# Optimization experiments

Measured on AMD Instinct MI355X. Metric: run time of the kernel, lower is better.

## Reference

```python
import jax, jax.numpy as jnp
import numpy as np

N_KERNELS = 5
MUL_FACTOR = 2.0


def setup_inputs() -> dict:
    key = jax.random.key(0)
    k1, k2 = jax.random.split(key)
    X = jax.random.normal(k1, (4096, 512), dtype=jnp.float32)
    Y = jax.random.normal(k2, (4096, 512), dtype=jnp.float32)
    return {"X": X, "Y": Y}


def _mmd(X, Y):
    # multipliers: 2.0 ** (arange(5) - 2) = [0.25, 0.5, 1, 2, 4]
    mults = MUL_FACTOR ** (jnp.arange(N_KERNELS, dtype=jnp.float32) - N_KERNELS // 2)
    Z = jnp.concatenate([X, Y], axis=0)            # [N+M, D]
    n = Z.shape[0]
    # squared euclidean pairwise distances (cdist ** 2)
    sq = jnp.sum(Z * Z, axis=-1)                    # [N+M]
    D2 = sq[:, None] + sq[None, :] - 2.0 * (Z @ Z.T)
    D2 = jnp.maximum(D2, 0.0)                       # [N+M, N+M]
    # bandwidth from detached distances: sum / (n^2 - n)
    bw = jax.lax.stop_gradient(jnp.sum(D2)) / (n * n - n)
    # multi-bandwidth RBF sum over kernels
    K = jnp.sum(jnp.exp(-D2[None, :, :] / (bw * mults)[:, None, None]), axis=0)
    Nx = X.shape[0]
    XX = jnp.mean(K[:Nx, :Nx])
    XY = jnp.mean(K[:Nx, Nx:])
    YY = jnp.mean(K[Nx:, Nx:])
    return XX - 2.0 * XY + YY


def reference(X, Y):
    return _mmd(X, Y)
```

## Files before the change

kernel.cpp:

```cpp
#include <hip/hip_runtime.h>

#define N_ROWS 8192
#define NX     4096
#define DIM    512
#define BT     128
#define NT     64
#define NTRI   2080
#define BK     32
#define NPERS  768

typedef __bf16 bf16_t;
typedef bf16_t bf16x8 __attribute__((ext_vector_type(8)));
typedef float  f32x4  __attribute__((ext_vector_type(4)));

#if __has_builtin(__builtin_amdgcn_exp2f)
  #define EXP2F __builtin_amdgcn_exp2f
#else
  #define EXP2F exp2f
#endif


__device__ __forceinline__ const float* zrow(const float* X, const float* Y, int r) {
    return (r < NX) ? (X + (size_t)r * DIM) : (Y + (size_t)(r - NX) * DIM);
}

__device__ __forceinline__ void gload_lds16(const bf16_t* g, bf16_t* l) {
    __builtin_amdgcn_global_load_lds(
        (__attribute__((address_space(1))) void*)(void*)(g),
        (__attribute__((address_space(3))) void*)(void*)(l), 16, 0, 0);
}

__global__ void k_prep(const float* __restrict__ X, const float* __restrict__ Y,
                       bf16_t* __restrict__ Zh, float* __restrict__ sqrow,
                       float* __restrict__ colsum, unsigned* __restrict__ tk1,
                       double* __restrict__ S1acc) {
    int t = threadIdx.x;
    if (blockIdx.x == 0) {
        colsum[t] = 0.f; colsum[t + 256] = 0.f;
        if (t == 0) { *tk1 = 0u; *S1acc = 0.0; }
    }
    int wv = t >> 6, lane = t & 63;
    int row = blockIdx.x * 4 + wv;
    const float4* z4 = (const float4*)zrow(X, Y, row);
    float4 a = z4[lane * 2], b = z4[lane * 2 + 1];
    bf16x8 h;
    h[0] = (bf16_t)a.x; h[1] = (bf16_t)a.y; h[2] = (bf16_t)a.z; h[3] = (bf16_t)a.w;
    h[4] = (bf16_t)b.x; h[5] = (bf16_t)b.y; h[6] = (bf16_t)b.z; h[7] = (bf16_t)b.w;
    *(bf16x8*)(Zh + (size_t)row * DIM + lane * 8) = h;
    float s = a.x*a.x + a.y*a.y + a.z*a.z + a.w*a.w
            + b.x*b.x + b.y*b.y + b.z*b.z + b.w*b.w;
    #pragma unroll
    for (int off = 32; off > 0; off >>= 1) s += __shfl_down(s, off);
    if (lane == 0) sqrow[row] = s;
}

__global__ __launch_bounds__(512) void k_colsum(const bf16_t* __restrict__ Zh,
                                                const float* __restrict__ sqrow,
                                                float* __restrict__ colsum,
                                                float* __restrict__ cvals,
                                                double* __restrict__ S1acc,
                                                unsigned* __restrict__ tk1,
                                                double* __restrict__ acc,
                                                unsigned* __restrict__ tk2) {
    __shared__ float red[8][4][8];
    __shared__ double dred[512];
    __shared__ int is_last;
    int t = threadIdx.x, lane = t & 63, wv = t >> 6;
    int n16 = lane & 15, q16 = lane >> 4;
    int g = blockIdx.x & 15, slab = blockIdx.x >> 4;
    int c0 = g * 32 + q16 * 8;
    float s[8] = {0.f, 0.f, 0.f, 0.f, 0.f, 0.f, 0.f, 0.f};
    #pragma unroll
    for (int it = 0; it < 8; ++it) {
        int r = slab * 1024 + it * 128 + wv * 16 + n16;
        bf16x8 v = *(const bf16x8*)(Zh + (size_t)r * DIM + c0);
        #pragma unroll
        for (int j = 0; j < 8; ++j) s[j] += (float)v[j];
    }
    #pragma unroll
    for (int off = 8; off >= 1; off >>= 1)
        #pragma unroll
        for (int j = 0; j < 8; ++j) s[j] += __shfl_down(s[j], off);
    if (n16 == 0)
        #pragma unroll
        for (int j = 0; j < 8; ++j) red[wv][q16][j] = s[j];
    __syncthreads();
    float oldc = 0.f;
    if (t < 32) {
        int q = t >> 3, j = t & 7;
        float v = 0.f;
        #pragma unroll
        for (int w = 0; w < 8; ++w) v += red[w][q][j];
        oldc = atomicAdd(&colsum[g * 32 + q * 8 + j], v);
    }
    double olds = 0.0;
    if (g == 0) {
        int i = slab * 1024 + t;
        double d = (double)sqrow[i] + (double)sqrow[i + 512];
        #pragma unroll
        for (int off = 32; off > 0; off >>= 1) d += __shfl_down(d, off);
        if (lane == 0) olds = atomicAdd(S1acc, d);
    }
    asm volatile("" :: "v"(oldc), "v"(olds));
    asm volatile("s_waitcnt vmcnt(0)" ::: "memory");
    __syncthreads();
    if (t == 0) is_last = (atomicAdd(tk1, 1u) == 127u);
    __syncthreads();
    if (!is_last) return;
    float cv = atomicAdd(&colsum[t], 0.f);
    dred[t] = (double)cv * (double)cv;
    __syncthreads();
    for (int off = 256; off > 0; off >>= 1) {
        if (t < off) dred[t] += dred[t + off];
        __syncthreads();
    }
    if (t < 8) acc[t * 16] = 0.0;
    if (t == 0) {
        double S1 = atomicAdd(S1acc, 0.0);
        double n = (double)N_ROWS;
        double sumD2 = 2.0 * n * S1 - 2.0 * dred[0];
        double bw = sumD2 / (n * n - n);
        const double LOG2E = 1.4426950408889634;
        double mult = 0.25;
        for (int k = 0; k < 5; ++k) {
            cvals[k] = (float)(-LOG2E / (bw * mult));
            mult *= 2.0;
        }
        *tk2 = 0u;
    }
}

__global__ __launch_bounds__(256, 3) void k_pair(const bf16_t* __restrict__ Zh,
                                                 const float* __restrict__ sqrow,
                                                 const float* __restrict__ cvals,
                                                 double* __restrict__ acc,
                                                 unsigned* __restrict__ tk2,
                                                 float* __restrict__ out) {
    int b = blockIdx.x;
    int ntile = (b < NTRI - 2 * NPERS) ? 3 : 2;
    int tis[3], tjs[3];
    #pragma unroll
    for (int g = 0; g < 3; ++g) {
        int T = b + g * NPERS;
        int ti_ = 0, tj_ = 0;
        if (T < NTRI) {
            int q = (T & 7) * (NTRI / 8) + (T >> 3);
            int I = 0, rem = q;
            #pragma unroll
            for (int it = 0; it < 8; ++it) {
                int rowcnt = 36 + (7 - I) * 64;
                if (rem >= rowcnt && I < 7) { rem -= rowcnt; ++I; } else break;
            }
            if (rem < 36) {
                int a = 0;
                #pragma unroll
                for (int it = 0; it < 7; ++it) {
                    int nxt = (a + 1) * 8 - (a + 1) * a / 2;
                    if (nxt <= rem) ++a; else break;
                }
                int off = a * 8 - a * (a - 1) / 2;
                ti_ = I * 8 + a;
                tj_ = I * 8 + a + (rem - off);
            } else {
                int r2 = rem - 36;
                int J = I + 1 + (r2 >> 6);
                int w = r2 & 63;
                ti_ = I * 8 + (w >> 3);
                tj_ = J * 8 + (w & 7);
            }
        }
        tis[g] = ti_; tjs[g] = tj_;
    }

    __shared__ bf16_t As[3][4096];
    __shared__ bf16_t Bs[3][4096];
    __shared__ float wsum[4];

    int t = threadIdx.x, lane = t & 63, wv = t >> 6;
    int wr = wv >> 1, wc = wv & 1;
    int n16 = lane & 15, q16 = lane >> 4;

    int r0_, q0_, r1_, q1_;
    { int c0 = t;       r0_ = c0 >> 2; q0_ = (c0 & 3) ^ ((r0_ >> 1) & 3);
      int c1 = 256 + t; r1_ = c1 >> 2; q1_ = (c1 & 3) ^ ((r1_ >> 1) & 3); }
    int ldsoff0 = (wv * 64) * 8;
    int ldsoff1 = (256 + wv * 64) * 8;

    int aoff[4], boff[4];
    #pragma unroll
    for (int aa = 0; aa < 4; ++aa) {
        int r = 16 * (wr * 4 + aa) + n16;
        aoff[aa] = (r * 4 + (q16 ^ ((r >> 1) & 3))) * 8;
    }
    #pragma unroll
    for (int bb = 0; bb < 4; ++bb) {
        int r = 16 * (wc * 4 + bb) + n16;
        boff[bb] = (r * 4 + (q16 ^ ((r >> 1) & 3))) * 8;
    }

    float c4 = cvals[4];

#define SETPTRS(TI, TJ, A0, B0, A1, B1) do {                        \
        (A0) = Zh + (size_t)((TI) * BT + r0_) * DIM + q0_ * 8;      \
        (B0) = Zh + (size_t)((TJ) * BT + r0_) * DIM + q0_ * 8;      \
        (A1) = Zh + (size_t)((TI) * BT + r1_) * DIM + q1_ * 8;      \
        (B1) = Zh + (size_t)((TJ) * BT + r1_) * DIM + q1_ * 8;      \
    } while (0)

#define STAGEP(A0, B0, A1, B1, KN, BUF) do {                        \
        gload_lds16((A0) + (KN), &As[BUF][ldsoff0]);                \
        gload_lds16((B0) + (KN), &Bs[BUF][ldsoff0]);                \
        gload_lds16((A1) + (KN), &As[BUF][ldsoff1]);                \
        gload_lds16((B1) + (KN), &Bs[BUF][ldsoff1]);                \
    } while (0)

#define WAITBAR(VM) do {                                            \
        asm volatile("s_waitcnt vmcnt(" VM ")" ::: "memory");       \
        __builtin_amdgcn_s_barrier();                               \
        __builtin_amdgcn_sched_barrier(0);                          \
    } while (0)

#define DOMFMA(RB) do {                                             \
        const bf16_t* Ab = &As[RB][0];                              \
        const bf16_t* Bb = &Bs[RB][0];                              \
        bf16x8 av[4], bv[4];                                        \
        _Pragma("unroll")                                           \
        for (int aa = 0; aa < 4; ++aa) av[aa] = *(const bf16x8*)(Ab + aoff[aa]); \
        _Pragma("unroll")                                           \
        for (int bb = 0; bb < 4; ++bb) bv[bb] = *(const bf16x8*)(Bb + boff[bb]); \
        __builtin_amdgcn_s_setprio(1);                              \
        _Pragma("unroll")                                           \
        for (int aa = 0; aa < 4; ++aa)                              \
            _Pragma("unroll")                                       \
            for (int bb = 0; bb < 4; ++bb)                          \
                accf[aa][bb] = __builtin_amdgcn_mfma_f32_16x16x32_bf16( \
                    av[aa], bv[bb], accf[aa][bb], 0, 0, 0);         \
        __builtin_amdgcn_s_setprio(0);                              \
    } while (0)

    const bf16_t *cA0, *cB0, *cA1, *cB1;
    SETPTRS(tis[0], tjs[0], cA0, cB0, cA1, cB1);
    STAGEP(cA0, cB0, cA1, cB1, 0, 0);
    STAGEP(cA0, cB0, cA1, cB1, BK, 1);

    #pragma unroll
    for (int g = 0; g < 3; ++g) {
        if (g >= ntile) break;
        int has_next = (g + 1 < ntile);
        const bf16_t *nA0 = cA0, *nB0 = cB0, *nA1 = cA1, *nB1 = cB1;
        if (has_next) SETPTRS(tis[g + 1], tjs[g + 1], nA0, nB0, nA1, nB1);

        f32x4 accf[4][4];
        #pragma unroll
        for (int a = 0; a < 4; ++a)
            #pragma unroll
            for (int bb = 0; bb < 4; ++bb)
                accf[a][bb] = (f32x4){0.f, 0.f, 0.f, 0.f};

        int rb = g % 3;
        const bf16_t *pA0 = cA0 + 2 * BK, *pB0 = cB0 + 2 * BK;
        const bf16_t *pA1 = cA1 + 2 * BK, *pB1 = cB1 + 2 * BK;
        for (int s = 0; s < 14; ++s) {
            WAITBAR("4");
            int wb = rb + 2; if (wb >= 3) wb -= 3;
            STAGEP(pA0, pB0, pA1, pB1, 0, wb);
            pA0 += BK; pB0 += BK; pA1 += BK; pB1 += BK;
            DOMFMA(rb);
            ++rb; if (rb == 3) rb = 0;
        }
        WAITBAR("4");
        if (has_next) STAGEP(nA0, nB0, nA1, nB1, 0, (g + 1) % 3);
        DOMFMA((g + 2) % 3);
        if (has_next) {
            WAITBAR("4");
            STAGEP(nA0, nB0, nA1, nB1, BK, (g + 2) % 3);
        } else {
            WAITBAR("0");
        }
        DOMFMA(g % 3);

        int i0 = tis[g] * BT + wr * 64;
        int j0 = tjs[g] * BT + wc * 64;
        float sqi[4][4], sqj[4];
        #pragma unroll
        for (int aa = 0; aa < 4; ++aa)
            #pragma unroll
            for (int r = 0; r < 4; ++r)
                sqi[aa][r] = sqrow[i0 + 16 * aa + q16 * 4 + r];
        #pragma unroll
        for (int bb = 0; bb < 4; ++bb)
            sqj[bb] = sqrow[j0 + 16 * bb + n16];

        float s_local = 0.f;
        #pragma unroll
        for (int aa = 0; aa < 4; ++aa) {
            #pragma unroll
            for (int bb = 0; bb < 4; ++bb) {
                #pragma unroll
                for (int r = 0; r < 4; ++r) {
                    float d2 = fmaf(-2.f, accf[aa][bb][r], sqi[aa][r] + sqj[bb]);
                    d2 = fmaxf(d2, 0.f);
                    float e4 = EXP2F(d2 * c4);
                    float e3 = e4 * e4;
                    float e2 = e3 * e3;
                    float e1 = e2 * e2;
                    float e0 = e1 * e1;
                    s_local += e4 + e3 + e2 + e1 + e0;
                }
            }
        }
        #pragma unroll
        for (int off = 32; off > 0; off >>= 1) s_local += __shfl_down(s_local, off);
        if (lane == 0) wsum[wv] = s_local;
        __syncthreads();
        if (t == 0) {
            float bs = wsum[0] + wsum[1] + wsum[2] + wsum[3];
            double si = (tis[g] < NT / 2) ? 1.0 : -1.0;
            double sj = (tjs[g] < NT / 2) ? 1.0 : -1.0;
            double w = si * sj * ((tis[g] == tjs[g]) ? 1.0 : 2.0);
            double oldv = atomicAdd(&acc[(b & 7) * 16], w * (double)bs);
            asm volatile("" :: "v"(oldv));
        }
        if (has_next) { cA0 = nA0; cB0 = nB0; cA1 = nA1; cB1 = nB1; }
    }

    if (t == 0) {
        asm volatile("s_waitcnt vmcnt(0)" ::: "memory");
        unsigned old = atomicAdd(tk2, 1u);
        if (old == NPERS - 1) {
            double ssum = 0.0;
            #pragma unroll
            for (int i = 0; i < 8; ++i) ssum += atomicAdd(&acc[i * 16], 0.0);
            out[0] = (float)(ssum / ((double)NX * (double)NX));
        }
    }
#undef SETPTRS
#undef STAGEP
#undef WAITBAR
#undef DOMFMA
}

extern "C" void kernel_launch(void* const* d_in, const int* in_sizes, int n_in,
                              void* d_out, int out_size, void* d_ws, size_t ws_size,
                              hipStream_t stream) {
    const float* X = (const float*)d_in[0];
    const float* Y = (const float*)d_in[1];
    float* out = (float*)d_out;

    float*    sqrow  = (float*)d_ws;
    float*    colsum = sqrow + 8192;
    float*    cvals  = (float*)((char*)d_ws + 34816);
    unsigned* tk1    = (unsigned*)((char*)d_ws + 34840);
    unsigned* tk2    = (unsigned*)((char*)d_ws + 34844);
    double*   S1acc  = (double*)((char*)d_ws + 34848);
    double*   acc    = (double*)((char*)d_ws + 34944);
    bf16_t*   Zh     = (bf16_t*)((char*)d_ws + 36864);

    k_prep  <<<2048, 256, 0, stream>>>(X, Y, Zh, sqrow, colsum, tk1, S1acc);
    k_colsum<<<128, 512, 0, stream>>>(Zh, sqrow, colsum, cvals, S1acc, tk1, acc, tk2);
    k_pair  <<<NPERS, 256, 0, stream>>>(Zh, sqrow, cvals, acc, tk2, out);
}
```

Baseline: 132.2 us.

## Fuse column-sum bandwidth reduction into pair kernel with dynamic tile queue

Removes the separate k_colsum launch and folds its column-sum and bandwidth computation into the first 128 blocks of k_pair. Those blocks publish the exp coefficients through a flag that other blocks spin-wait on before the epilogue, so the GEMM main loop can overlap with the reduction. Static three-tiles-per-block assignment is replaced by an atomic work queue so persistent blocks pull tiles dynamically for better load balance. The cost is extra per-tile atomics and barriers, a spin-wait that depends on all 128 reducer blocks being co-resident, and a possible deadlock if they are not.

```diff
diff --git a/kernel.cpp b/kernel.cpp
--- a/kernel.cpp
+++ b/kernel.cpp
@@ -30,14 +30,42 @@
         (__attribute__((address_space(3))) void*)(void*)(l), 16, 0, 0);
 }
 
+__device__ __forceinline__ void decode_tile(int T, int* pti, int* ptj) {
+    int q = (T & 7) * (NTRI / 8) + (T >> 3);
+    int I = 0, rem = q;
+    #pragma unroll
+    for (int it = 0; it < 8; ++it) {
+        int rowcnt = 36 + (7 - I) * 64;
+        if (rem >= rowcnt && I < 7) { rem -= rowcnt; ++I; } else break;
+    }
+    if (rem < 36) {
+        int a = 0;
+        #pragma unroll
+        for (int it = 0; it < 7; ++it) {
+            int nxt = (a + 1) * 8 - (a + 1) * a / 2;
+            if (nxt <= rem) ++a; else break;
+        }
+        int off = a * 8 - a * (a - 1) / 2;
+        *pti = I * 8 + a;
+        *ptj = I * 8 + a + (rem - off);
+    } else {
+        int r2 = rem - 36;
+        int J = I + 1 + (r2 >> 6);
+        int w = r2 & 63;
+        *pti = I * 8 + (w >> 3);
+        *ptj = J * 8 + (w & 7);
+    }
+}
+
 __global__ void k_prep(const float* __restrict__ X, const float* __restrict__ Y,
                        bf16_t* __restrict__ Zh, float* __restrict__ sqrow,
                        float* __restrict__ colsum, unsigned* __restrict__ tk1,
-                       double* __restrict__ S1acc) {
+                       unsigned* __restrict__ tk2, double* __restrict__ S1acc,
+                       unsigned* __restrict__ wq, unsigned* __restrict__ flag) {
     int t = threadIdx.x;
     if (blockIdx.x == 0) {
         colsum[t] = 0.f; colsum[t + 256] = 0.f;
-        if (t == 0) { *tk1 = 0u; *S1acc = 0.0; }
+        if (t == 0) { *tk1 = 0u; *tk2 = 0u; *S1acc = 0.0; *wq = NPERS; *flag = 0u; }
     }
     int wv = t >> 6, lane = t & 63;
     int row = blockIdx.x * 4 + wv;
@@ -54,138 +82,110 @@
     if (lane == 0) sqrow[row] = s;
 }
 
-__global__ __launch_bounds__(512) void k_colsum(const bf16_t* __restrict__ Zh,
-                                                const float* __restrict__ sqrow,
-                                                float* __restrict__ colsum,
-                                                float* __restrict__ cvals,
-                                                double* __restrict__ S1acc,
-                                                unsigned* __restrict__ tk1,
-                                                double* __restrict__ acc,
-                                                unsigned* __restrict__ tk2) {
-    __shared__ float red[8][4][8];
-    __shared__ double dred[512];
-    __shared__ int is_last;
-    int t = threadIdx.x, lane = t & 63, wv = t >> 6;
-    int n16 = lane & 15, q16 = lane >> 4;
-    int g = blockIdx.x & 15, slab = blockIdx.x >> 4;
-    int c0 = g * 32 + q16 * 8;
-    float s[8] = {0.f, 0.f, 0.f, 0.f, 0.f, 0.f, 0.f, 0.f};
-    #pragma unroll
-    for (int it = 0; it < 8; ++it) {
-        int r = slab * 1024 + it * 128 + wv * 16 + n16;
-        bf16x8 v = *(const bf16x8*)(Zh + (size_t)r * DIM + c0);
-        #pragma unroll
-        for (int j = 0; j < 8; ++j) s[j] += (float)v[j];
-    }
-    #pragma unroll
-    for (int off = 8; off >= 1; off >>= 1)
-        #pragma unroll
-        for (int j = 0; j < 8; ++j) s[j] += __shfl_down(s[j], off);
-    if (n16 == 0)
-        #pragma unroll
-        for (int j = 0; j < 8; ++j) red[wv][q16][j] = s[j];
-    __syncthreads();
-    float oldc = 0.f;
-    if (t < 32) {
-        int q = t >> 3, j = t & 7;
-        float v = 0.f;
-        #pragma unroll
-        for (int w = 0; w < 8; ++w) v += red[w][q][j];
-        oldc = atomicAdd(&colsum[g * 32 + q * 8 + j], v);
-    }
-    double olds = 0.0;
-    if (g == 0) {
-        int i = slab * 1024 + t;
-        double d = (double)sqrow[i] + (double)sqrow[i + 512];
-        #pragma unroll
-        for (int off = 32; off > 0; off >>= 1) d += __shfl_down(d, off);
-        if (lane == 0) olds = atomicAdd(S1acc, d);
-    }
-    asm volatile("" :: "v"(oldc), "v"(olds));
-    asm volatile("s_waitcnt vmcnt(0)" ::: "memory");
-    __syncthreads();
-    if (t == 0) is_last = (atomicAdd(tk1, 1u) == 127u);
-    __syncthreads();
-    if (!is_last) return;
-    float cv = atomicAdd(&colsum[t], 0.f);
-    dred[t] = (double)cv * (double)cv;
-    __syncthreads();
-    for (int off = 256; off > 0; off >>= 1) {
-        if (t < off) dred[t] += dred[t + off];
-        __syncthreads();
-    }
-    if (t < 8) acc[t * 16] = 0.0;
-    if (t == 0) {
-        double S1 = atomicAdd(S1acc, 0.0);
-        double n = (double)N_ROWS;
-        double sumD2 = 2.0 * n * S1 - 2.0 * dred[0];
-        double bw = sumD2 / (n * n - n);
-        const double LOG2E = 1.4426950408889634;
-        double mult = 0.25;
-        for (int k = 0; k < 5; ++k) {
-            cvals[k] = (float)(-LOG2E / (bw * mult));
-            mult *= 2.0;
-        }
-        *tk2 = 0u;
-    }
-}
-
 __global__ __launch_bounds__(256, 3) void k_pair(const bf16_t* __restrict__ Zh,
                                                  const float* __restrict__ sqrow,
-                                                 const float* __restrict__ cvals,
+                                                 float* __restrict__ colsum,
+                                                 float* __restrict__ cvals,
+                                                 double* __restrict__ S1acc,
+                                                 unsigned* __restrict__ tk1,
+                                                 unsigned* __restrict__ wq,
+                                                 unsigned* __restrict__ flag,
                                                  double* __restrict__ acc,
                                                  unsigned* __restrict__ tk2,
                                                  float* __restrict__ out) {
     int b = blockIdx.x;
-    int ntile = (b < NTRI - 2 * NPERS) ? 3 : 2;
-    int tis[3], tjs[3];
-    #pragma unroll
-    for (int g = 0; g < 3; ++g) {
-        int T = b + g * NPERS;
-        int ti_ = 0, tj_ = 0;
-        if (T < NTRI) {
-            int q = (T & 7) * (NTRI / 8) + (T >> 3);
-            int I = 0, rem = q;
-            #pragma unroll
-            for (int it = 0; it < 8; ++it) {
-                int rowcnt = 36 + (7 - I) * 64;
-                if (rem >= rowcnt && I < 7) { rem -= rowcnt; ++I; } else break;
-            }
-            if (rem < 36) {
-                int a = 0;
-                #pragma unroll
-                for (int it = 0; it < 7; ++it) {
-                    int nxt = (a + 1) * 8 - (a + 1) * a / 2;
-                    if (nxt <= rem) ++a; else break;
-                }
-                int off = a * 8 - a * (a - 1) / 2;
-                ti_ = I * 8 + a;
-                tj_ = I * 8 + a + (rem - off);
-            } else {
-                int r2 = rem - 36;
-                int J = I + 1 + (r2 >> 6);
-                int w = r2 & 63;
-                ti_ = I * 8 + (w >> 3);
-                tj_ = J * 8 + (w & 7);
-            }
-        }
-        tis[g] = ti_; tjs[g] = tj_;
-    }
-
     __shared__ bf16_t As[3][4096];
     __shared__ bf16_t Bs[3][4096];
     __shared__ float wsum[4];
+    __shared__ int   lds_next;
+    __shared__ float lds_c4;
 
     int t = threadIdx.x, lane = t & 63, wv = t >> 6;
-    int wr = wv >> 1, wc = wv & 1;
     int n16 = lane & 15, q16 = lane >> 4;
+
+    if (b < 128) {
+        float* red = (float*)&Bs[0][0];
+        double* dred = (double*)&As[0][0];
+        int g = b & 15, slab = b >> 4;
+        int c0 = g * 32 + q16 * 8;
+        float s[8] = {0.f,0.f,0.f,0.f,0.f,0.f,0.f,0.f};
+        for (int it = 0; it < 16; ++it) {
+            int r = slab * 1024 + it * 64 + wv * 16 + n16;
+            bf16x8 v = *(const bf16x8*)(Zh + (size_t)r * DIM + c0);
+            #pragma unroll
+            for (int j = 0; j < 8; ++j) s[j] += (float)v[j];
+        }
+        #pragma unroll
+        for (int off = 8; off >= 1; off >>= 1)
+            #pragma unroll
+            for (int j = 0; j < 8; ++j) s[j] += __shfl_down(s[j], off);
+        if (n16 == 0)
+            #pragma unroll
+            for (int j = 0; j < 8; ++j) red[(wv * 4 + q16) * 8 + j] = s[j];
+        __syncthreads();
+        float oldc = 0.f;
+        if (t < 32) {
+            int q = t >> 3, j = t & 7;
+            float v = 0.f;
+            #pragma unroll
+            for (int w = 0; w < 4; ++w) v += red[(w * 4 + q) * 8 + j];
+            oldc = atomicAdd(&colsum[g * 32 + q * 8 + j], v);
+        }
+        double olds = 0.0;
+        if (g == 0) {
+            int i = slab * 1024 + t;
+            double d = (double)sqrow[i] + (double)sqrow[i + 256]
+                     + (double)sqrow[i + 512] + (double)sqrow[i + 768];
+            #pragma unroll
+            for (int off = 32; off > 0; off >>= 1) d += __shfl_down(d, off);
+            if (lane == 0) olds = atomicAdd(S1acc, d);
+        }
+        asm volatile("" :: "v"(oldc), "v"(olds));
+        asm volatile("s_waitcnt vmcnt(0)" ::: "memory");
+        __syncthreads();
+        __shared__ int is_last;
+        if (t == 0) is_last = (atomicAdd(tk1, 1u) == 127u);
+        __syncthreads();
+        if (is_last) {
+            float cv0 = atomicAdd(&colsum[t], 0.f);
+            float cv1 = atomicAdd(&colsum[t + 256], 0.f);
+            dred[t] = (double)cv0 * cv0 + (double)cv1 * cv1;
+            __syncthreads();
+            for (int off = 128; off > 0; off >>= 1) {
+                if (t < off) dred[t] += dred[t + off];
+                __syncthreads();
+            }
+            if (t < 8) {
+                unsigned long long o =
+                    atomicExch((unsigned long long*)&acc[t * 16], 0ull);
+                asm volatile("" :: "v"(o));
+            }
+            if (t == 0) {
+                double S1 = atomicAdd(S1acc, 0.0);
+                double n = (double)N_ROWS;
+                double bw = (2.0 * n * S1 - 2.0 * dred[0]) / (n * n - n);
+                const double LOG2E = 1.4426950408889634;
+                double mult = 0.25;
+                float olda = 0.f;
+                for (int k = 0; k < 5; ++k) {
+                    olda += atomicExch(&cvals[k], (float)(-LOG2E / (bw * mult)));
+                    mult *= 2.0;
+                }
+                asm volatile("" :: "v"(olda));
+                asm volatile("s_waitcnt vmcnt(0)" ::: "memory");
+                unsigned of = atomicExch(flag, 1u);
+                asm volatile("" :: "v"(of));
+            }
+            __syncthreads();
+        }
+    }
 
     int r0_, q0_, r1_, q1_;
     { int c0 = t;       r0_ = c0 >> 2; q0_ = (c0 & 3) ^ ((r0_ >> 1) & 3);
       int c1 = 256 + t; r1_ = c1 >> 2; q1_ = (c1 & 3) ^ ((r1_ >> 1) & 3); }
     int ldsoff0 = (wv * 64) * 8;
     int ldsoff1 = (256 + wv * 64) * 8;
-
+    int wr = wv >> 1, wc = wv & 1;
     int aoff[4], boff[4];
     #pragma unroll
     for (int aa = 0; aa < 4; ++aa) {
@@ -197,8 +197,6 @@
         int r = 16 * (wc * 4 + bb) + n16;
         boff[bb] = (r * 4 + (q16 ^ ((r >> 1) & 3))) * 8;
     }
-
-    float c4 = cvals[4];
 
 #define SETPTRS(TI, TJ, A0, B0, A1, B1) do {                        \
         (A0) = Zh + (size_t)((TI) * BT + r0_) * DIM + q0_ * 8;      \
@@ -206,20 +204,17 @@
         (A1) = Zh + (size_t)((TI) * BT + r1_) * DIM + q1_ * 8;      \
         (B1) = Zh + (size_t)((TJ) * BT + r1_) * DIM + q1_ * 8;      \
     } while (0)
-
 #define STAGEP(A0, B0, A1, B1, KN, BUF) do {                        \
         gload_lds16((A0) + (KN), &As[BUF][ldsoff0]);                \
         gload_lds16((B0) + (KN), &Bs[BUF][ldsoff0]);                \
         gload_lds16((A1) + (KN), &As[BUF][ldsoff1]);                \
         gload_lds16((B1) + (KN), &Bs[BUF][ldsoff1]);                \
     } while (0)
-
 #define WAITBAR(VM) do {                                            \
         asm volatile("s_waitcnt vmcnt(" VM ")" ::: "memory");       \
         __builtin_amdgcn_s_barrier();                               \
         __builtin_amdgcn_sched_barrier(0);                          \
     } while (0)
-
 #define DOMFMA(RB) do {                                             \
         const bf16_t* Ab = &As[RB][0];                              \
         const bf16_t* Bb = &Bs[RB][0];                              \
@@ -238,17 +233,26 @@
         __builtin_amdgcn_s_setprio(0);                              \
     } while (0)
 
+    int ti, tj;
+    decode_tile(b, &ti, &tj);
     const bf16_t *cA0, *cB0, *cA1, *cB1;
-    SETPTRS(tis[0], tjs[0], cA0, cB0, cA1, cB1);
+    SETPTRS(ti, tj, cA0, cB0, cA1, cB1);
     STAGEP(cA0, cB0, cA1, cB1, 0, 0);
     STAGEP(cA0, cB0, cA1, cB1, BK, 1);
 
-    #pragma unroll
-    for (int g = 0; g < 3; ++g) {
-        if (g >= ntile) break;
-        int has_next = (g + 1 < ntile);
+    int g3 = 0;
+    float c4 = 0.f;
+    int seen = 0;
+
+    for (;;) {
+        if (t == 0) lds_next = (int)atomicAdd(wq, 1u);
+        __syncthreads();
+        int nxt = lds_next;
+        int has_next = (nxt < NTRI);
+        int nti = 0, ntj = 0;
+        if (has_next) decode_tile(nxt, &nti, &ntj);
         const bf16_t *nA0 = cA0, *nB0 = cB0, *nA1 = cA1, *nB1 = cB1;
-        if (has_next) SETPTRS(tis[g + 1], tjs[g + 1], nA0, nB0, nA1, nB1);
+        if (has_next) SETPTRS(nti, ntj, nA0, nB0, nA1, nB1);
 
         f32x4 accf[4][4];
         #pragma unroll
@@ -257,7 +261,7 @@
             for (int bb = 0; bb < 4; ++bb)
                 accf[a][bb] = (f32x4){0.f, 0.f, 0.f, 0.f};
 
-        int rb = g % 3;
+        int rb = g3;
         const bf16_t *pA0 = cA0 + 2 * BK, *pB0 = cB0 + 2 * BK;
         const bf16_t *pA1 = cA1 + 2 * BK, *pB1 = cB1 + 2 * BK;
         for (int s = 0; s < 14; ++s) {
@@ -268,19 +272,35 @@
             DOMFMA(rb);
             ++rb; if (rb == 3) rb = 0;
         }
-        WAITBAR("4");
-        if (has_next) STAGEP(nA0, nB0, nA1, nB1, 0, (g + 1) % 3);
-        DOMFMA((g + 2) % 3);
-        if (has_next) {
+        {
             WAITBAR("4");
-            STAGEP(nA0, nB0, nA1, nB1, BK, (g + 2) % 3);
-        } else {
-            WAITBAR("0");
-        }
-        DOMFMA(g % 3);
-
-        int i0 = tis[g] * BT + wr * 64;
-        int j0 = tjs[g] * BT + wc * 64;
+            int b1 = g3 + 1; if (b1 >= 3) b1 -= 3;
+            if (has_next) STAGEP(nA0, nB0, nA1, nB1, 0, b1);
+            int b2 = g3 + 2; if (b2 >= 3) b2 -= 3;
+            DOMFMA(b2);
+        }
+        {
+            if (has_next) {
+                WAITBAR("4");
+                int b2 = g3 + 2; if (b2 >= 3) b2 -= 3;
+                STAGEP(nA0, nB0, nA1, nB1, BK, b2);
+            } else {
+                WAITBAR("0");
+            }
+            DOMFMA(g3);
+        }
+
+        if (!seen) {
+            if (t == 0) {
+                while (atomicAdd(flag, 0u) == 0u) __builtin_amdgcn_s_sleep(8);
+                lds_c4 = atomicAdd(&cvals[4], 0.f);
+            }
+            __syncthreads();
+            c4 = lds_c4;
+            seen = 1;
+        }
+        int i0 = ti * BT + wr * 64;
+        int j0 = tj * BT + wc * 64;
         float sqi[4][4], sqj[4];
         #pragma unroll
         for (int aa = 0; aa < 4; ++aa)
@@ -315,13 +335,16 @@
         __syncthreads();
         if (t == 0) {
             float bs = wsum[0] + wsum[1] + wsum[2] + wsum[3];
-            double si = (tis[g] < NT / 2) ? 1.0 : -1.0;
-            double sj = (tjs[g] < NT / 2) ? 1.0 : -1.0;
-            double w = si * sj * ((tis[g] == tjs[g]) ? 1.0 : 2.0);
+            double si = (ti < NT / 2) ? 1.0 : -1.0;
+            double sj = (tj < NT / 2) ? 1.0 : -1.0;
+            double w = si * sj * ((ti == tj) ? 1.0 : 2.0);
             double oldv = atomicAdd(&acc[(b & 7) * 16], w * (double)bs);
             asm volatile("" :: "v"(oldv));
         }
-        if (has_next) { cA0 = nA0; cB0 = nB0; cA1 = nA1; cB1 = nB1; }
+        if (!has_next) break;
+        ti = nti; tj = ntj;
+        cA0 = nA0; cB0 = nB0; cA1 = nA1; cB1 = nB1;
+        ++g3; if (g3 == 3) g3 = 0;
     }
 
     if (t == 0) {
@@ -353,10 +376,12 @@
     unsigned* tk1    = (unsigned*)((char*)d_ws + 34840);
     unsigned* tk2    = (unsigned*)((char*)d_ws + 34844);
     double*   S1acc  = (double*)((char*)d_ws + 34848);
+    unsigned* wq     = (unsigned*)((char*)d_ws + 34856);
+    unsigned* flag   = (unsigned*)((char*)d_ws + 34860);
     double*   acc    = (double*)((char*)d_ws + 34944);
     bf16_t*   Zh     = (bf16_t*)((char*)d_ws + 36864);
 
-    k_prep  <<<2048, 256, 0, stream>>>(X, Y, Zh, sqrow, colsum, tk1, S1acc);
-    k_colsum<<<128, 512, 0, stream>>>(Zh, sqrow, colsum, cvals, S1acc, tk1, acc, tk2);
-    k_pair  <<<NPERS, 256, 0, stream>>>(Zh, sqrow, cvals, acc, tk2, out);
-}
+    k_prep<<<2048, 256, 0, stream>>>(X, Y, Zh, sqrow, colsum, tk1, tk2, S1acc, wq, flag);
+    k_pair<<<NPERS, 256, 0, stream>>>(Zh, sqrow, colsum, cvals, S1acc, tk1, wq, flag,
+                                      acc, tk2, out);
+}
```

Measured after the change: 179.1 us. 1.35x slower.
